# Performance work log

Measured on AMD Instinct MI355X. Metric: run time of the kernel, lower is better.

The kernel has to match this reference:

```python
import jax, jax.numpy as jnp
import numpy as np

N_NODES = 50000
N_EDGES = 1600000
IN_CH = 128
HID_CH = 128
OUT_CH = 2
NUM_GRAPHS = 64
NUM_LAYERS = 3


def setup_inputs() -> dict:
    key = jax.random.key(0)
    ks = jax.random.split(key, 12)
    x = jax.random.normal(ks[0], (N_NODES, IN_CH), dtype=jnp.float32)
    edge_index = jax.random.randint(ks[1], (2, N_EDGES), 0, N_NODES, dtype=jnp.int64)
    batch = jnp.sort(jax.random.randint(ks[2], (N_NODES,), 0, NUM_GRAPHS, dtype=jnp.int64))
    s = 0.05
    W0 = jax.random.normal(ks[3], (IN_CH, HID_CH), dtype=jnp.float32) * s
    b0 = jnp.zeros((HID_CH,), dtype=jnp.float32)
    W1 = jax.random.normal(ks[4], (HID_CH, HID_CH), dtype=jnp.float32) * s
    b1 = jnp.zeros((HID_CH,), dtype=jnp.float32)
    W2 = jax.random.normal(ks[5], (HID_CH, HID_CH), dtype=jnp.float32) * s
    b2 = jnp.zeros((HID_CH,), dtype=jnp.float32)
    Wlin = jax.random.normal(ks[6], (HID_CH, OUT_CH), dtype=jnp.float32) * s
    blin = jnp.zeros((OUT_CH,), dtype=jnp.float32)
    return {"x": x, "edge_index": edge_index, "batch": batch,
            "W0": W0, "b0": b0, "W1": W1, "b1": b1, "W2": W2, "b2": b2,
            "Wlin": Wlin, "blin": blin}


def _gcn_layer(h, src, dst, norm, W, b):
    # GCNConv: (D^-1/2 (A+I) D^-1/2) (h W) + b
    h = h @ W                               # [N, C]
    msg = h[src] * norm[:, None]            # [E+N, C] gather + scale
    agg = jax.ops.segment_sum(msg, dst, num_segments=N_NODES)  # scatter-add
    return agg + b


def reference(x, edge_index, batch, W0, b0, W1, b1, W2, b2, Wlin, blin):
    loops = jnp.arange(N_NODES, dtype=edge_index.dtype)
    src = jnp.concatenate([edge_index[0], loops])
    dst = jnp.concatenate([edge_index[1], loops])
    deg = jax.ops.segment_sum(jnp.ones_like(dst, dtype=x.dtype), dst,
                              num_segments=N_NODES)
    dis = jax.lax.rsqrt(deg)                # deg >= 1 due to self loops
    norm = dis[src] * dis[dst]              # [E+N]

    h = x
    for W, b in ((W0, b0), (W1, b1), (W2, b2)):
        h = jax.nn.relu(_gcn_layer(h, src, dst, norm, W, b))

    # global mean pool over graphs
    sums = jax.ops.segment_sum(h, batch, num_segments=NUM_GRAPHS)
    cnts = jax.ops.segment_sum(jnp.ones((N_NODES,), dtype=h.dtype), batch,
                               num_segments=NUM_GRAPHS)
    pooled = sums / jnp.maximum(cnts, 1.0)[:, None]  # [G, HID]
    return pooled @ Wlin + blin                       # [G, OUT]
```

## Files before the change

### kernel.cpp

```cpp
#include <hip/hip_runtime.h>
#include <hip/hip_fp16.h>

#define N_NODES   50000
#define N_EDGES   1600000
#define CH        128
#define OUTC      2
#define NGRAPHS   64

#define NBUCK     391
#define EPB       4096
#define F1BLOCKS  391
#define BCAP      5120

#define GR        64


__global__ __launch_bounds__(256) void bhist_k(const int* __restrict__ dst,
                                               int* __restrict__ bhist) {
    __shared__ int hist[NBUCK];
    const int tid = threadIdx.x;
    const int e0  = blockIdx.x * EPB;
    const int nE  = min(EPB, N_EDGES - e0);
    for (int i = tid; i < NBUCK; i += 256) hist[i] = 0;
    __syncthreads();
    for (int i = tid; i < nE; i += 256) atomicAdd(&hist[dst[e0 + i] >> 7], 1);
    __syncthreads();
    for (int i = tid; i < NBUCK; i += 256) if (hist[i]) atomicAdd(&bhist[i], hist[i]);
}

__global__ __launch_bounds__(512) void bscan_k(const int* __restrict__ bhist,
                                               int* __restrict__ bbase,
                                               int* __restrict__ bcur) {
    const int t = threadIdx.x, lane = t & 63, w = t >> 6;
    int v = (t < NBUCK) ? bhist[t] : 0;
    int iv = v;
    #pragma unroll
    for (int d = 1; d < 64; d <<= 1) {
        int o = __shfl_up(iv, d, 64);
        if (lane >= d) iv += o;
    }
    __shared__ int ws[8];
    if (lane == 63) ws[w] = iv;
    __syncthreads();
    int add = 0;
    #pragma unroll
    for (int k = 0; k < 8; k++) if (k < w) add += ws[k];
    int excl = add + iv - v;
    if (t < NBUCK) { bbase[t] = excl; bcur[t] = excl; }
    if (t == NBUCK - 1) bbase[NBUCK] = excl + v;
}

__global__ __launch_bounds__(256) void bucket_scatter_k(const int* __restrict__ src,
                                                        const int* __restrict__ dst,
                                                        int* __restrict__ bucketCursor,
                                                        int2* __restrict__ stage) {
    __shared__ int hist[NBUCK];
    __shared__ int cur[NBUCK];
    __shared__ int gbase[NBUCK];
    const int tid = threadIdx.x;
    const int e0  = blockIdx.x * EPB;
    const int nE  = min(EPB, N_EDGES - e0);

    for (int i = tid; i < NBUCK; i += 256) hist[i] = 0;
    __syncthreads();
    for (int i = tid; i < nE; i += 256) {
        int d = dst[e0 + i];
        atomicAdd(&hist[d >> 7], 1);
    }
    __syncthreads();
    for (int i = tid; i < NBUCK; i += 256) {
        int h = hist[i];
        gbase[i] = h ? atomicAdd(&bucketCursor[i], h) : 0;
        cur[i] = 0;
    }
    __syncthreads();
    for (int i = tid; i < nE; i += 256) {
        int d = dst[e0 + i];
        int s = src[e0 + i];
        int b = d >> 7;
        int pos = gbase[b] + atomicAdd(&cur[b], 1);
        stage[pos] = make_int2(s, d);
    }
}

__global__ __launch_bounds__(256) void bucket_build_k(const int2* __restrict__ stage,
                                                      const int* __restrict__ bbase,
                                                      int* __restrict__ offsets,
                                                      float* __restrict__ dis,
                                                      int* __restrict__ csr) {
    __shared__ int lcnt[128];
    __shared__ int lcur[128];
    __shared__ int wtot[2];
    __shared__ int loc[BCAP];
    const int tid    = threadIdx.x;
    const int b      = blockIdx.x;
    const int first  = b << 7;
    const int nNodes = min(128, N_NODES - first);
    const int base   = bbase[b];
    const int bsize  = bbase[b + 1] - base;

    if (tid < 128) lcnt[tid] = 0;
    __syncthreads();
    for (int i = tid; i < bsize; i += 256)
        atomicAdd(&lcnt[stage[base + i].y - first], 1);
    __syncthreads();

    int iv = 0, c = 0;
    if (tid < 128) {
        c = lcnt[tid];
        iv = c;
        #pragma unroll
        for (int d = 1; d < 64; d <<= 1) {
            int o = __shfl_up(iv, d, 64);
            if ((tid & 63) >= d) iv += o;
        }
        if ((tid & 63) == 63) wtot[tid >> 6] = iv;
    }
    __syncthreads();
    if (tid < 128) {
        int add  = (tid >= 64) ? wtot[0] : 0;
        int excl = add + iv - c;
        lcur[tid] = excl;
        if (tid < nNodes) {
            offsets[first + tid] = base + excl;
            dis[first + tid]     = rsqrtf((float)(c + 1));
        }
    }
    if (b == NBUCK - 1 && tid == 0) offsets[N_NODES] = base + bsize;
    __syncthreads();

    if (bsize <= BCAP) {
        for (int i = tid; i < bsize; i += 256) {
            int2 sd = stage[base + i];
            int pos = atomicAdd(&lcur[sd.y - first], 1);
            loc[pos] = sd.x;
        }
        __syncthreads();
        for (int i = tid; i < bsize; i += 256) csr[base + i] = loc[i];
    } else {
        for (int i = tid; i < bsize; i += 256) {
            int2 sd = stage[base + i];
            int pos = atomicAdd(&lcur[sd.y - first], 1);
            csr[base + pos] = sd.x;
        }
    }
}

__global__ __launch_bounds__(256) void boundary_k(const int* __restrict__ batch,
                                                  int* __restrict__ gstart) {
    int i = blockIdx.x * 256 + threadIdx.x;
    if (i >= N_NODES) return;
    int bc = batch[i];
    if (i == 0) {
        for (int g = 0; g <= bc; g++) gstart[g] = 0;
    } else {
        int bp = batch[i - 1];
        for (int g = bp + 1; g <= bc; g++) gstart[g] = i;
    }
    if (i == N_NODES - 1) {
        for (int g = bc + 1; g <= NGRAPHS; g++) gstart[g] = N_NODES;
    }
}

struct alignas(16) H8 { __half2 a, b, c, d; };

__global__ __launch_bounds__(128) void gemm_scale_k(const float* __restrict__ h,
                                                    const float* __restrict__ W,
                                                    const float* __restrict__ dis,
                                                    __half* __restrict__ out) {
    __shared__ float Hl[GR][36];
    __shared__ float Wl[32][CH];
    const int tid = threadIdx.x;
    const int tx  = tid & 15;
    const int ty  = tid >> 4;
    const int rowBase = blockIdx.x * GR;

    float acc[8][8];
    #pragma unroll
    for (int j = 0; j < 8; j++)
        #pragma unroll
        for (int i = 0; i < 8; i++) acc[j][i] = 0.f;

    for (int kt = 0; kt < 4; kt++) {
        __syncthreads();
        #pragma unroll
        for (int i = 0; i < 4; i++) {
            int f = tid + i * 128;
            int r = f >> 3;
            int q = f & 7;
            int n = rowBase + r;
            float4 v = make_float4(0.f, 0.f, 0.f, 0.f);
            if (n < N_NODES) v = *(const float4*)&h[(size_t)n * CH + kt * 32 + q * 4];
            *(float4*)&Hl[r][q * 4] = v;
        }
        #pragma unroll
        for (int i = 0; i < 8; i++) {
            int f  = tid + i * 128;
            int kr = f >> 5;
            int c4 = (f & 31) * 4;
            *(float4*)&Wl[kr][c4] = *(const float4*)&W[(size_t)(kt * 32 + kr) * CH + c4];
        }
        __syncthreads();

        #pragma unroll
        for (int k4 = 0; k4 < 8; k4++) {
            float4 hreg[8];
            #pragma unroll
            for (int j = 0; j < 8; j++)
                hreg[j] = *(float4*)&Hl[ty * 8 + j][k4 * 4];
            #pragma unroll
            for (int kk = 0; kk < 4; kk++) {
                float4 w0 = *(float4*)&Wl[k4 * 4 + kk][tx * 8];
                float4 w1 = *(float4*)&Wl[k4 * 4 + kk][tx * 8 + 4];
                #pragma unroll
                for (int j = 0; j < 8; j++) {
                    float hv = ((float*)&hreg[j])[kk];
                    acc[j][0] += hv * w0.x; acc[j][1] += hv * w0.y;
                    acc[j][2] += hv * w0.z; acc[j][3] += hv * w0.w;
                    acc[j][4] += hv * w1.x; acc[j][5] += hv * w1.y;
                    acc[j][6] += hv * w1.z; acc[j][7] += hv * w1.w;
                }
            }
        }
    }

    #pragma unroll
    for (int j = 0; j < 8; j++) {
        int n = rowBase + ty * 8 + j;
        if (n < N_NODES) {
            float s = dis[n];
            H8 o;
            o.a = __floats2half2_rn(acc[j][0] * s, acc[j][1] * s);
            o.b = __floats2half2_rn(acc[j][2] * s, acc[j][3] * s);
            o.c = __floats2half2_rn(acc[j][4] * s, acc[j][5] * s);
            o.d = __floats2half2_rn(acc[j][6] * s, acc[j][7] * s);
            *(H8*)&out[(size_t)n * CH + tx * 8] = o;
        }
    }
}

__global__ __launch_bounds__(256) void agg_k(const __half* __restrict__ hs,
                                             const int* __restrict__ offsets,
                                             const int* __restrict__ csr,
                                             const float* __restrict__ dis,
                                             const float* __restrict__ bias,
                                             float* __restrict__ out) {
    const __half2* hs2 = (const __half2*)hs;
    const int wid  = threadIdx.x >> 6;
    const int lane = threadIdx.x & 63;
    const int n = blockIdx.x * 4 + wid;
    if (n >= N_NODES) return;

    float ax[8], ay[8];
    #pragma unroll
    for (int j = 0; j < 8; j++) { ax[j] = 0.f; ay[j] = 0.f; }

    {
        float2 v = __half22float2(hs2[(size_t)n * 64 + lane]);
        ax[0] = v.x; ay[0] = v.y;
    }

    const int beg = offsets[n];
    const int end = offsets[n + 1];
    int e = beg;
    for (; e + 8 <= end; e += 8) {
        int idx[8];
        #pragma unroll
        for (int j = 0; j < 8; j++) idx[j] = csr[e + j];
        __half2 v[8];
        #pragma unroll
        for (int j = 0; j < 8; j++) v[j] = hs2[(size_t)idx[j] * 64 + lane];
        #pragma unroll
        for (int j = 0; j < 8; j++) {
            float2 f = __half22float2(v[j]);
            ax[j] += f.x; ay[j] += f.y;
        }
    }
    for (; e < end; e++) {
        int s = csr[e];
        float2 f = __half22float2(hs2[(size_t)s * 64 + lane]);
        ax[0] += f.x; ay[0] += f.y;
    }

    #pragma unroll
    for (int j = 0; j < 4; j++) { ax[j] += ax[j + 4]; ay[j] += ay[j + 4]; }
    #pragma unroll
    for (int j = 0; j < 2; j++) { ax[j] += ax[j + 2]; ay[j] += ay[j + 2]; }
    float sx = ax[0] + ax[1];
    float sy = ay[0] + ay[1];

    const float dn = dis[n];
    float2 b = *(const float2*)&bias[lane * 2];
    float2 r;
    r.x = fmaxf(dn * sx + b.x, 0.f);
    r.y = fmaxf(dn * sy + b.y, 0.f);
    *(float2*)&out[(size_t)n * CH + lane * 2] = r;
}

__global__ __launch_bounds__(256) void pool_k(const float* __restrict__ h,
                                              const int* __restrict__ gstart,
                                              float* __restrict__ gsum) {
    const int g   = blockIdx.y;
    const int s   = blockIdx.x;
    const int tid = threadIdx.x;
    const int r   = tid >> 5;
    const int cq  = tid & 31;
    const int start = gstart[g], end = gstart[g + 1];
    const int len   = end - start;
    const int chunk = (len + 7) >> 3;
    const int lo = start + s * chunk;
    const int hi = min(lo + chunk, end);

    float4 acc = make_float4(0.f, 0.f, 0.f, 0.f);
    for (int row = lo + r; row < hi; row += 8) {
        float4 v = *(const float4*)&h[(size_t)row * CH + cq * 4];
        acc.x += v.x; acc.y += v.y; acc.z += v.z; acc.w += v.w;
    }

    __shared__ float4 red[256];
    red[tid] = acc;
    __syncthreads();
    #pragma unroll
    for (int off = 4; off >= 1; off >>= 1) {
        if (r < off) {
            float4 o = red[tid + off * 32];
            red[tid].x += o.x; red[tid].y += o.y;
            red[tid].z += o.z; red[tid].w += o.w;
        }
        __syncthreads();
    }
    if (r == 0) {
        float4 v = red[tid];
        atomicAdd(&gsum[g * CH + cq * 4 + 0], v.x);
        atomicAdd(&gsum[g * CH + cq * 4 + 1], v.y);
        atomicAdd(&gsum[g * CH + cq * 4 + 2], v.z);
        atomicAdd(&gsum[g * CH + cq * 4 + 3], v.w);
    }
}

__global__ __launch_bounds__(128) void head_k(const float* __restrict__ gsum,
                                              const int* __restrict__ gstart,
                                              const float* __restrict__ Wlin,
                                              const float* __restrict__ blin,
                                              float* __restrict__ out) {
    const int t = threadIdx.x;
    const int g = t >> 1;
    const int o = t & 1;
    float cnt = (float)max(gstart[g + 1] - gstart[g], 1);
    float s = 0.f;
    for (int ci = 0; ci < CH; ci++) s += gsum[g * CH + ci] * Wlin[ci * OUTC + o];
    out[g * OUTC + o] = s / cnt + blin[o];
}


static inline size_t alignup(size_t x) { return (x + 255) & ~(size_t)255; }

extern "C" void kernel_launch(void* const* d_in, const int* in_sizes, int n_in,
                              void* d_out, int out_size, void* d_ws, size_t ws_size,
                              hipStream_t stream) {
    const float* x     = (const float*)d_in[0];
    const int*   eidx  = (const int*)d_in[1];
    const int*   batch = (const int*)d_in[2];
    const float* W0    = (const float*)d_in[3];
    const float* b0    = (const float*)d_in[4];
    const float* W1    = (const float*)d_in[5];
    const float* b1    = (const float*)d_in[6];
    const float* W2    = (const float*)d_in[7];
    const float* b2    = (const float*)d_in[8];
    const float* Wlin  = (const float*)d_in[9];
    const float* blin  = (const float*)d_in[10];
    float* out = (float*)d_out;

    const int* src = eidx;
    const int* dst = eidx + N_EDGES;

    char* p = (char*)d_ws;
    int*    offsets = (int*)p;     p += alignup((N_NODES + 1) * 4);
    float*  dis     = (float*)p;   p += alignup(N_NODES * 4);
    int*    bhist   = (int*)p;     p += alignup(NBUCK * 4);
    int*    bbase   = (int*)p;     p += alignup((NBUCK + 1) * 4);
    int*    bcur    = (int*)p;     p += alignup(NBUCK * 4);
    int*    gstart  = (int*)p;     p += alignup((NGRAPHS + 1) * 4);
    int*    csr     = (int*)p;     p += alignup((size_t)N_EDGES * 4);
    float*  bufA    = (float*)p;   p += alignup((size_t)N_NODES * CH * 4);
    __half* hsbuf   = (__half*)p;  p += alignup((size_t)N_NODES * CH * 2);
    float*  gsum    = (float*)p;   p += alignup(NGRAPHS * CH * 4);

    int2* stage = (int2*)bufA;

    hipMemsetAsync(bhist, 0, NBUCK * 4, stream);
    hipMemsetAsync(gsum, 0, NGRAPHS * CH * 4, stream);

    bhist_k<<<F1BLOCKS, 256, 0, stream>>>(dst, bhist);
    bscan_k<<<1, 512, 0, stream>>>(bhist, bbase, bcur);
    bucket_scatter_k<<<F1BLOCKS, 256, 0, stream>>>(src, dst, bcur, stage);
    bucket_build_k<<<NBUCK, 256, 0, stream>>>(stage, bbase, offsets, dis, csr);
    boundary_k<<<(N_NODES + 255) / 256, 256, 0, stream>>>(batch, gstart);

    const int GB = (N_NODES + GR - 1) / GR;
    const int AB = (N_NODES + 3) / 4;

    gemm_scale_k<<<GB, 128, 0, stream>>>(x, W0, dis, hsbuf);
    agg_k<<<AB, 256, 0, stream>>>(hsbuf, offsets, csr, dis, b0, bufA);
    gemm_scale_k<<<GB, 128, 0, stream>>>(bufA, W1, dis, hsbuf);
    agg_k<<<AB, 256, 0, stream>>>(hsbuf, offsets, csr, dis, b1, bufA);
    gemm_scale_k<<<GB, 128, 0, stream>>>(bufA, W2, dis, hsbuf);
    agg_k<<<AB, 256, 0, stream>>>(hsbuf, offsets, csr, dis, b2, bufA);

    pool_k<<<dim3(8, NGRAPHS), 256, 0, stream>>>(bufA, gstart, gsum);
    head_k<<<1, 128, 0, stream>>>(gsum, gstart, Wlin, blin, out);
}
```

Measured before the change: 331.1 us.

## Use MFMA fp16 GEMM and store layer activations in half precision

Replaces the FP32 SIMT register-tiled GEMM with a kernel built on the 16x16x32 f16 MFMA instruction. Weights are pre-transposed and converted to half once per call. The aggregation output between layers is now stored as fp16, which halves GEMM input reads and pool reads. The edge staging buffer gets its own workspace region instead of aliasing bufA. This costs precision in the intermediate activations and the GEMM inputs, plus an extra small prep kernel.

```diff
diff --git a/kernel.cpp b/kernel.cpp
--- a/kernel.cpp
+++ b/kernel.cpp
@@ -13,6 +13,9 @@
 #define BCAP      5120
 
 #define GR        64
+
+using f16x8 = __attribute__((ext_vector_type(8))) _Float16;
+using f32x4 = __attribute__((ext_vector_type(4))) float;
 
 
 __global__ __launch_bounds__(256) void bhist_k(const int* __restrict__ dst,
@@ -162,79 +165,98 @@
     }
 }
 
-struct alignas(16) H8 { __half2 a, b, c, d; };
-
-__global__ __launch_bounds__(128) void gemm_scale_k(const float* __restrict__ h,
-                                                    const float* __restrict__ W,
-                                                    const float* __restrict__ dis,
-                                                    __half* __restrict__ out) {
-    __shared__ float Hl[GR][36];
-    __shared__ float Wl[32][CH];
+__global__ __launch_bounds__(256) void prep_w_k(const float* __restrict__ W0,
+                                                const float* __restrict__ W1,
+                                                const float* __restrict__ W2,
+                                                __half* __restrict__ T0,
+                                                __half* __restrict__ T1,
+                                                __half* __restrict__ T2) {
+    const float* W = (blockIdx.x == 0) ? W0 : (blockIdx.x == 1) ? W1 : W2;
+    __half* Wt     = (blockIdx.x == 0) ? T0 : (blockIdx.x == 1) ? T1 : T2;
+    for (int i = threadIdx.x; i < CH * CH; i += 256) {
+        int k = i >> 7, c = i & 127;
+        Wt[c * CH + k] = __float2half(W[i]);
+    }
+}
+
+template <bool F32IN>
+__global__ __launch_bounds__(256) void gemm_mfma_k(const void* __restrict__ hin,
+                                                   const __half* __restrict__ Wt,
+                                                   const float* __restrict__ dis,
+                                                   __half* __restrict__ out) {
+    __shared__ _Float16 Hl[GR][136];
+    __shared__ _Float16 Wl[CH][136];
     const int tid = threadIdx.x;
-    const int tx  = tid & 15;
-    const int ty  = tid >> 4;
     const int rowBase = blockIdx.x * GR;
 
-    float acc[8][8];
-    #pragma unroll
-    for (int j = 0; j < 8; j++)
-        #pragma unroll
-        for (int i = 0; i < 8; i++) acc[j][i] = 0.f;
-
+    {
+        const int c = tid >> 1, q = tid & 1;
+        #pragma unroll
+        for (int i = 0; i < 8; i++)
+            *(f16x8*)&Wl[c][q * 64 + i * 8] =
+                *(const f16x8*)&Wt[c * CH + q * 64 + i * 8];
+    }
+    {
+        const int r = tid >> 2, q = tid & 3;
+        const int n = rowBase + r;
+        if constexpr (F32IN) {
+            const float* h = (const float*)hin;
+            #pragma unroll
+            for (int i = 0; i < 8; i++) {
+                float4 v = make_float4(0.f, 0.f, 0.f, 0.f);
+                if (n < N_NODES) v = *(const float4*)&h[(size_t)n * CH + q * 32 + i * 4];
+                *(__half2*)&Hl[r][q * 32 + i * 4]     = __floats2half2_rn(v.x, v.y);
+                *(__half2*)&Hl[r][q * 32 + i * 4 + 2] = __floats2half2_rn(v.z, v.w);
+            }
+        } else {
+            const _Float16* h = (const _Float16*)hin;
+            #pragma unroll
+            for (int i = 0; i < 4; i++) {
+                f16x8 v = {};
+                if (n < N_NODES) v = *(const f16x8*)&h[(size_t)n * CH + q * 32 + i * 8];
+                *(f16x8*)&Hl[r][q * 32 + i * 8] = v;
+            }
+        }
+    }
+    __syncthreads();
+
+    const int w = tid >> 6, lane = tid & 63;
+    const int l15 = lane & 15, kg = lane >> 4;
+
+    f32x4 acc[8];
+    #pragma unroll
+    for (int t = 0; t < 8; t++) acc[t] = (f32x4){0.f, 0.f, 0.f, 0.f};
+
+    #pragma unroll
     for (int kt = 0; kt < 4; kt++) {
-        __syncthreads();
-        #pragma unroll
-        for (int i = 0; i < 4; i++) {
-            int f = tid + i * 128;
-            int r = f >> 3;
-            int q = f & 7;
-            int n = rowBase + r;
-            float4 v = make_float4(0.f, 0.f, 0.f, 0.f);
-            if (n < N_NODES) v = *(const float4*)&h[(size_t)n * CH + kt * 32 + q * 4];
-            *(float4*)&Hl[r][q * 4] = v;
-        }
-        #pragma unroll
-        for (int i = 0; i < 8; i++) {
-            int f  = tid + i * 128;
-            int kr = f >> 5;
-            int c4 = (f & 31) * 4;
-            *(float4*)&Wl[kr][c4] = *(const float4*)&W[(size_t)(kt * 32 + kr) * CH + c4];
-        }
-        __syncthreads();
-
-        #pragma unroll
-        for (int k4 = 0; k4 < 8; k4++) {
-            float4 hreg[8];
+        f16x8 a = *(f16x8*)&Hl[w * 16 + l15][kt * 32 + kg * 8];
+        #pragma unroll
+        for (int t = 0; t < 8; t++) {
+            f16x8 b = *(f16x8*)&Wl[t * 16 + l15][kt * 32 + kg * 8];
+            acc[t] = __builtin_amdgcn_mfma_f32_16x16x32_f16(a, b, acc[t], 0, 0, 0);
+        }
+    }
+    __syncthreads();
+
+    #pragma unroll
+    for (int r = 0; r < 4; r++) {
+        const int lrow = w * 16 + kg * 4 + r;
+        const int n = rowBase + lrow;
+        const float s = (n < N_NODES) ? dis[n] : 0.f;
+        #pragma unroll
+        for (int t = 0; t < 8; t++)
+            Hl[lrow][t * 16 + l15] = (_Float16)(acc[t][r] * s);
+    }
+    __syncthreads();
+
+    {
+        const int r = tid >> 2, q = tid & 3;
+        const int n = rowBase + r;
+        if (n < N_NODES) {
             #pragma unroll
-            for (int j = 0; j < 8; j++)
-                hreg[j] = *(float4*)&Hl[ty * 8 + j][k4 * 4];
-            #pragma unroll
-            for (int kk = 0; kk < 4; kk++) {
-                float4 w0 = *(float4*)&Wl[k4 * 4 + kk][tx * 8];
-                float4 w1 = *(float4*)&Wl[k4 * 4 + kk][tx * 8 + 4];
-                #pragma unroll
-                for (int j = 0; j < 8; j++) {
-                    float hv = ((float*)&hreg[j])[kk];
-                    acc[j][0] += hv * w0.x; acc[j][1] += hv * w0.y;
-                    acc[j][2] += hv * w0.z; acc[j][3] += hv * w0.w;
-                    acc[j][4] += hv * w1.x; acc[j][5] += hv * w1.y;
-                    acc[j][6] += hv * w1.z; acc[j][7] += hv * w1.w;
-                }
-            }
-        }
-    }
-
-    #pragma unroll
-    for (int j = 0; j < 8; j++) {
-        int n = rowBase + ty * 8 + j;
-        if (n < N_NODES) {
-            float s = dis[n];
-            H8 o;
-            o.a = __floats2half2_rn(acc[j][0] * s, acc[j][1] * s);
-            o.b = __floats2half2_rn(acc[j][2] * s, acc[j][3] * s);
-            o.c = __floats2half2_rn(acc[j][4] * s, acc[j][5] * s);
-            o.d = __floats2half2_rn(acc[j][6] * s, acc[j][7] * s);
-            *(H8*)&out[(size_t)n * CH + tx * 8] = o;
+            for (int i = 0; i < 4; i++)
+                *(f16x8*)&((_Float16*)out)[(size_t)n * CH + q * 32 + i * 8] =
+                    *(f16x8*)&Hl[r][q * 32 + i * 8];
         }
     }
 }
@@ -244,7 +266,7 @@
                                              const int* __restrict__ csr,
                                              const float* __restrict__ dis,
                                              const float* __restrict__ bias,
-                                             float* __restrict__ out) {
+                                             __half* __restrict__ out) {
     const __half2* hs2 = (const __half2*)hs;
     const int wid  = threadIdx.x >> 6;
     const int lane = threadIdx.x & 63;
@@ -291,15 +313,15 @@
 
     const float dn = dis[n];
     float2 b = *(const float2*)&bias[lane * 2];
-    float2 r;
-    r.x = fmaxf(dn * sx + b.x, 0.f);
-    r.y = fmaxf(dn * sy + b.y, 0.f);
-    *(float2*)&out[(size_t)n * CH + lane * 2] = r;
-}
-
-__global__ __launch_bounds__(256) void pool_k(const float* __restrict__ h,
+    float rx = fmaxf(dn * sx + b.x, 0.f);
+    float ry = fmaxf(dn * sy + b.y, 0.f);
+    ((__half2*)out)[(size_t)n * 64 + lane] = __floats2half2_rn(rx, ry);
+}
+
+__global__ __launch_bounds__(256) void pool_k(const __half* __restrict__ h,
                                               const int* __restrict__ gstart,
                                               float* __restrict__ gsum) {
+    const __half2* h2 = (const __half2*)h;
     const int g   = blockIdx.y;
     const int s   = blockIdx.x;
     const int tid = threadIdx.x;
@@ -313,8 +335,9 @@
 
     float4 acc = make_float4(0.f, 0.f, 0.f, 0.f);
     for (int row = lo + r; row < hi; row += 8) {
-        float4 v = *(const float4*)&h[(size_t)row * CH + cq * 4];
-        acc.x += v.x; acc.y += v.y; acc.z += v.z; acc.w += v.w;
+        float2 a = __half22float2(h2[(size_t)row * 64 + cq * 2]);
+        float2 b = __half22float2(h2[(size_t)row * 64 + cq * 2 + 1]);
+        acc.x += a.x; acc.y += a.y; acc.z += b.x; acc.w += b.y;
     }
 
     __shared__ float4 red[256];
@@ -382,11 +405,13 @@
     int*    bcur    = (int*)p;     p += alignup(NBUCK * 4);
     int*    gstart  = (int*)p;     p += alignup((NGRAPHS + 1) * 4);
     int*    csr     = (int*)p;     p += alignup((size_t)N_EDGES * 4);
-    float*  bufA    = (float*)p;   p += alignup((size_t)N_NODES * CH * 4);
+    __half* Wt0     = (__half*)p;  p += alignup(CH * CH * 2);
+    __half* Wt1     = (__half*)p;  p += alignup(CH * CH * 2);
+    __half* Wt2     = (__half*)p;  p += alignup(CH * CH * 2);
+    __half* bufA    = (__half*)p;  p += alignup((size_t)N_NODES * CH * 2);
     __half* hsbuf   = (__half*)p;  p += alignup((size_t)N_NODES * CH * 2);
+    int2*   stage   = (int2*)p;    p += alignup((size_t)N_EDGES * 8);
     float*  gsum    = (float*)p;   p += alignup(NGRAPHS * CH * 4);
-
-    int2* stage = (int2*)bufA;
 
     hipMemsetAsync(bhist, 0, NBUCK * 4, stream);
     hipMemsetAsync(gsum, 0, NGRAPHS * CH * 4, stream);
@@ -396,15 +421,16 @@
     bucket_scatter_k<<<F1BLOCKS, 256, 0, stream>>>(src, dst, bcur, stage);
     bucket_build_k<<<NBUCK, 256, 0, stream>>>(stage, bbase, offsets, dis, csr);
     boundary_k<<<(N_NODES + 255) / 256, 256, 0, stream>>>(batch, gstart);
+    prep_w_k<<<3, 256, 0, stream>>>(W0, W1, W2, Wt0, Wt1, Wt2);
 
     const int GB = (N_NODES + GR - 1) / GR;
     const int AB = (N_NODES + 3) / 4;
 
-    gemm_scale_k<<<GB, 128, 0, stream>>>(x, W0, dis, hsbuf);
+    gemm_mfma_k<true><<<GB, 256, 0, stream>>>(x, Wt0, dis, hsbuf);
     agg_k<<<AB, 256, 0, stream>>>(hsbuf, offsets, csr, dis, b0, bufA);
-    gemm_scale_k<<<GB, 128, 0, stream>>>(bufA, W1, dis, hsbuf);
+    gemm_mfma_k<false><<<GB, 256, 0, stream>>>(bufA, Wt1, dis, hsbuf);
     agg_k<<<AB, 256, 0, stream>>>(hsbuf, offsets, csr, dis, b1, bufA);
-    gemm_scale_k<<<GB, 128, 0, stream>>>(bufA, W2, dis, hsbuf);
+    gemm_mfma_k<false><<<GB, 256, 0, stream>>>(bufA, Wt2, dis, hsbuf);
     agg_k<<<AB, 256, 0, stream>>>(hsbuf, offsets, csr, dis, b2, bufA);
 
     pool_k<<<dim3(8, NGRAPHS), 256, 0, stream>>>(bufA, gstart, gsum);
```

Result: faster. 307.5 us (-7.1%).
